# Optimization experiments

Measured on AMD Instinct MI355X. Metric: run time of the kernel, lower is better.

Reference implementation:

```python
import math
import jax, jax.numpy as jnp
from jax import lax
import numpy as np

B, N, D, H, L, F = 128, 200, 128, 8, 3, 2048


def setup_inputs():
    key = jax.random.key(0)
    ks = jax.random.split(key, 24)
    g = lambda i, shape: (0.05 * jax.random.normal(ks[i], shape)).astype(jnp.float32)
    coords = jax.random.uniform(ks[0], (B, N, 2), dtype=jnp.float32)
    demands = jax.random.uniform(ks[1], (B, N), minval=1.0, maxval=10.0, dtype=jnp.float32)
    demands = demands.at[:, 0].set(0.0)  # depot demand = 0
    capacity = jnp.full((B,), 50.0, jnp.float32)
    return dict(
        coords=coords, demands_raw=demands, capacity_raw=capacity,
        embed_W=g(2, (D, 3)), embed_b=g(3, (D,)),
        Wqkv=g(4, (L, 3 * D, D)), bqkv=g(5, (L, 3 * D)),
        Wo=g(6, (L, D, D)), bo=g(7, (L, D)),
        W1=g(8, (L, F, D)), b1=g(9, (L, F)),
        W2=g(10, (L, D, F)), b2=g(11, (L, D)),
        ln1_g=jnp.ones((L, D), jnp.float32), ln1_b=jnp.zeros((L, D), jnp.float32),
        ln2_g=jnp.ones((L, D), jnp.float32), ln2_b=jnp.zeros((L, D), jnp.float32),
        Wq=g(12, (D, D)), Wk=g(13, (D, D)),
        Wcap=g(14, (D, 1)), bcap=g(15, (D,)),
        Wctx=g(16, (D, 3 * D)), bctx=g(17, (D,)),
    )


def _ln(x, g, b):
    m = x.mean(-1, keepdims=True)
    v = ((x - m) ** 2).mean(-1, keepdims=True)
    return (x - m) / jnp.sqrt(v + 1e-5) * g + b


def _forward(coords, demands_raw, capacity_raw, embed_W, embed_b, Wqkv, bqkv, Wo, bo,
             W1, b1, W2, b2, ln1_g, ln1_b, ln2_g, ln2_b, Wq, Wk, Wcap, bcap, Wctx, bctx):
    Bd, Nd, _ = coords.shape
    cap = capacity_raw.reshape(Bd, 1)
    demand_ratio = demands_raw / cap                       # (B,N)
    x = jnp.concatenate([coords, demand_ratio[..., None]], -1)  # (B,N,3)
    h = x @ embed_W.T + embed_b                            # (B,N,D)
    d = h.shape[-1]
    dh = d // H
    # --- transformer encoder (post-LN, relu FFN), eval mode (no dropout) ---
    for i in range(Wqkv.shape[0]):
        qkv = h @ Wqkv[i].T + bqkv[i]
        q, k, v = jnp.split(qkv, 3, -1)
        q = q.reshape(Bd, Nd, H, dh)
        k = k.reshape(Bd, Nd, H, dh)
        v = v.reshape(Bd, Nd, H, dh)
        s = jnp.einsum('bqhd,bkhd->bhqk', q, k) / math.sqrt(dh)
        a = jax.nn.softmax(s, -1)
        o = jnp.einsum('bhqk,bkhd->bqhd', a, v).reshape(Bd, Nd, d) @ Wo[i].T + bo[i]
        h = _ln(h + o, ln1_g[i], ln1_b[i])
        f = jax.nn.relu(h @ W1[i].T + b1[i]) @ W2[i].T + b2[i]
        h = _ln(h + f, ln2_g[i], ln2_b[i])
    global_ctx = h.mean(1)                                 # (B,D)
    kmat = h @ Wk.T                                        # K cache: static across steps
    sqrt_d = math.sqrt(d)
    max_steps = 2 * (Nd - 1) + 1
    ar = jnp.arange(Bd)

    def step(carry, _):
        current, visited, remaining, done, key = carry
        key, sk = jax.random.split(key)
        cur_h = h[ar, current]                             # (B,D)
        cap_h = remaining @ Wcap.T + bcap                  # (B,D)
        q_in = jnp.concatenate([cur_h, global_ctx, cap_h], -1)
        q = (q_in @ Wctx.T + bctx) @ Wq.T                  # (B,D)
        logits = (kmat * q[:, None, :]).sum(-1) / sqrt_d   # (B,N)
        infeasible = visited | (demand_ratio > remaining)
        feas_cust = (~visited[:, 1:]) & (demand_ratio[:, 1:] <= remaining)
        has_feas = feas_cust.any(1)
        all_served = visited[:, 1:].all(1)
        force_depot = all_served & (current != 0) & (~done)
        at_depot = (current == 0) & (~done)
        not_depot = (current != 0) & (~done)
        # prevent_early_return=True path
        depot_mask = (at_depot & has_feas) | (not_depot & has_feas & (~all_served))
        infeasible = infeasible.at[:, 0].set(infeasible[:, 0] | depot_mask)
        force_depot = force_depot | (not_depot & (~has_feas)) | done
        masked = jnp.where(infeasible, -1e9, logits)
        logp = jax.nn.log_softmax(masked, -1)
        sel = jax.random.categorical(sk, masked)           # sampling decode
        sel_logp = logp[ar, sel]
        sel = jnp.where(force_depot, 0, sel)
        sel_logp = jnp.where(force_depot, 0.0, sel_logp)
        is_depot = sel == 0
        take = demand_ratio[ar, sel][:, None]
        remaining = jnp.clip(jnp.where(is_depot[:, None], 1.0, remaining - take), 0.0, 1.0)
        visited = visited.at[ar, sel].set(visited[ar, sel] | (~is_depot))
        done = done | (visited[:, 1:].all(1) & (sel == 0))
        return (sel, visited, remaining, done, key), (sel, sel_logp)

    init = (jnp.zeros(Bd, jnp.int32), jnp.zeros((Bd, Nd), bool),
            jnp.ones((Bd, 1), coords.dtype), jnp.zeros(Bd, bool), jax.random.key(42))
    _, (acts, lps) = lax.scan(step, init, None, length=max_steps)
    path = jnp.concatenate([jnp.zeros((Bd, 1), jnp.int32), acts.T], 1)  # (B, 1+max_steps)
    logps = lps.sum(0)                                                  # (B,)
    return path, logps


def reference(coords, demands_raw, capacity_raw, embed_W, embed_b, Wqkv, bqkv, Wo, bo,
              W1, b1, W2, b2, ln1_g, ln1_b, ln2_g, ln2_b, Wq, Wk, Wcap, bcap, Wctx, bctx):
    return _forward(coords, demands_raw, capacity_raw, embed_W, embed_b, Wqkv, bqkv, Wo, bo,
                    W1, b1, W2, b2, ln1_g, ln1_b, ln2_g, ln2_b, Wq, Wk, Wcap, bcap, Wctx, bctx)
```

## Files before the change

### kernel.cpp

```cpp
#include <hip/hip_runtime.h>
#include <hip/hip_bf16.h>
#include <stdint.h>
#include <math.h>

#define NB 128
#define NN 200
#define ND 128
#define NH 8
#define DH 16
#define NL 3
#define NF 2048
#define NT (NB * NN)
#define NSTEP 399

__host__ __device__ inline void tf2x32(unsigned k0, unsigned k1, unsigned x0, unsigned x1,
                                       unsigned* o0, unsigned* o1) {
  unsigned ks[3] = {k0, k1, k0 ^ k1 ^ 0x1BD11BDAu};
  x0 += ks[0]; x1 += ks[1];
  const unsigned R[2][4] = {{13u, 15u, 26u, 6u}, {17u, 29u, 16u, 24u}};
#pragma unroll
  for (int i = 0; i < 5; ++i) {
#pragma unroll
    for (int j = 0; j < 4; ++j) {
      unsigned r = R[i & 1][j];
      x0 += x1;
      x1 = (x1 << r) | (x1 >> (32u - r));
      x1 ^= x0;
    }
    x0 += ks[(i + 1) % 3];
    x1 += ks[(i + 2) % 3] + (unsigned)(i + 1);
  }
  *o0 = x0; *o1 = x1;
}

__global__ void k_rng(unsigned* __restrict__ rng) {
  __shared__ unsigned ksh[2 * NSTEP];
  const int l = threadIdx.x;
  if (l == 0) {
    unsigned k0 = 0u, k1 = 42u;
    for (int t = 0; t < NSTEP; ++t) {
      ksh[2 * t] = k0; ksh[2 * t + 1] = k1;
      unsigned a0, a1;
      tf2x32(k0, k1, 0u, 0u, &a0, &a1);
      k0 = a0; k1 = a1;
    }
  }
  __syncthreads();
  for (int t = l; t < NSTEP; t += 64) {
    unsigned s0, s1;
    tf2x32(ksh[2 * t], ksh[2 * t + 1], 0u, 1u, &s0, &s1);
    rng[2 * t] = s0; rng[2 * t + 1] = s1;
  }
}

__global__ __launch_bounds__(256) void k_gum(const unsigned* __restrict__ rng, float* __restrict__ gum) {
  int idx = blockIdx.x * 256 + threadIdx.x;
  if (idx >= NSTEP * NT) return;
  int t = idx / NT, j = idx - t * NT;
  unsigned o0, o1;
  tf2x32(rng[2 * t], rng[2 * t + 1], 0u, (unsigned)j, &o0, &o1);
  unsigned bits = o0 ^ o1;
  float u01 = __uint_as_float((bits >> 9) | 0x3f800000u) - 1.0f;
  float uu = fmaxf(1.17549435082228751e-38f, u01);
  gum[idx] = (float)(-log(-log((double)uu)));
}

__global__ void k_tr(const float* __restrict__ src, float* __restrict__ dst, int R, int C) {
  int i = blockIdx.x * 256 + threadIdx.x;
  if (i >= R * C) return;
  int c = i / R, r = i - c * R;
  dst[i] = src[(size_t)r * C + c];
}

__global__ void k_trd(const float* __restrict__ src, double* __restrict__ dst, int R, int C) {
  int i = blockIdx.x * 256 + threadIdx.x;
  if (i >= R * C) return;
  int c = i / R, r = i - c * R;
  dst[i] = (double)src[(size_t)r * C + c];
}

__global__ void k_embed(const float* __restrict__ coords, const float* __restrict__ dem,
                        const float* __restrict__ cap, const float* __restrict__ eW,
                        const float* __restrict__ eb, float* __restrict__ h, float* __restrict__ dr) {
  int gid = blockIdx.x * blockDim.x + threadIdx.x;
  int t = gid >> 7, d = gid & 127;
  int b = t / NN;
  float drv = dem[t] / cap[b];
  double acc = (double)eW[d * 3] * (double)coords[2 * t]
             + (double)eW[d * 3 + 1] * (double)coords[2 * t + 1]
             + (double)eW[d * 3 + 2] * (double)drv;
  h[gid] = (float)acc + eb[d];
  if (d == 0) dr[t] = drv;
}

#define QT 8
__global__ __launch_bounds__(384) void k_qkv(const float* __restrict__ h, const double* __restrict__ WT,
                                             const float* __restrict__ bias, float* __restrict__ qkv) {
  const int t0 = blockIdx.x * QT, j = threadIdx.x;
  __shared__ double hsh[ND][QT];
  for (int idx = j; idx < ND * QT; idx += 384) {
    int t = idx & 7, k = idx >> 3;
    hsh[k][t] = (double)h[(size_t)(t0 + t) * ND + k];
  }
  __syncthreads();
  double acc[QT];
#pragma unroll
  for (int t = 0; t < QT; ++t) acc[t] = 0.0;
  for (int k = 0; k < ND; ++k) {
    double w = WT[(size_t)k * 384 + j];
#pragma unroll
    for (int t = 0; t < QT; ++t) acc[t] += w * hsh[k][t];
  }
  float bv = bias[j];
#pragma unroll
  for (int t = 0; t < QT; ++t)
    qkv[(size_t)(t0 + t) * 384 + j] = (float)acc[t] + bv;
}

__global__ __launch_bounds__(256) void k_attn(const float* __restrict__ qkv, float* __restrict__ att) {
  const int b = blockIdx.x / NH, hh = blockIdx.x % NH, tid = threadIdx.x;
  const int lane = tid & 63, w = tid >> 6;
  __shared__ float qsh[NN][DH + 1];
  __shared__ float ksh[NN][DH + 1];
  __shared__ float vsh[NN][DH + 1];
  __shared__ float ashw[4][NN + 8];
  for (int idx = tid; idx < NN * DH; idx += 256) {
    int n = idx / DH, d2 = idx % DH;
    size_t base = (size_t)(b * NN + n) * 384 + hh * DH + d2;
    qsh[n][d2] = qkv[base];
    ksh[n][d2] = qkv[base + ND];
    vsh[n][d2] = qkv[base + 2 * ND];
  }
  __syncthreads();
  const int dd = lane & 15, q4 = lane >> 4;
  for (int qn = w; qn < NN; qn += 4) {
    double qv[DH];
#pragma unroll
    for (int d = 0; d < DH; ++d) qv[d] = (double)qsh[qn][d];
    float sf[4];
#pragma unroll
    for (int s = 0; s < 4; ++s) {
      int n = lane + 64 * s;
      if (n < NN) {
        double a = 0.0;
#pragma unroll
        for (int d = 0; d < DH; ++d) a += qv[d] * (double)ksh[n][d];
        sf[s] = (float)a / 4.0f;
      } else sf[s] = -3.0e38f;
    }
    float m = fmaxf(fmaxf(sf[0], sf[1]), fmaxf(sf[2], sf[3]));
    for (int off = 1; off < 64; off <<= 1) m = fmaxf(m, __shfl_xor(m, off, 64));
    double e[4];
    double esum = 0.0;
#pragma unroll
    for (int s = 0; s < 4; ++s) {
      int n = lane + 64 * s;
      e[s] = (n < NN) ? exp((double)(sf[s] - m)) : 0.0;
      esum += e[s];
    }
    for (int off = 1; off < 64; off <<= 1) esum += __shfl_xor(esum, off, 64);
#pragma unroll
    for (int s = 0; s < 4; ++s) {
      int n = lane + 64 * s;
      if (n < NN) ashw[w][n] = (float)(e[s] / esum);
    }
    double o = 0.0;
    for (int i = 0; i < 50; ++i) {
      int n = q4 * 50 + i;
      o += (double)ashw[w][n] * (double)vsh[n][dd];
    }
    o += __shfl_xor(o, 16, 64);
    o += __shfl_xor(o, 32, 64);
    if (lane < DH)
      att[(size_t)(b * NN + qn) * ND + hh * DH + lane] = (float)o;
  }
}

#define OT 4
__global__ __launch_bounds__(128) void k_oln(const float* __restrict__ att, const double* __restrict__ WoT,
                                             const float* __restrict__ bo, const float* __restrict__ g,
                                             const float* __restrict__ bb, const float* __restrict__ h,
                                             double* __restrict__ h64T) {
  const int t0 = blockIdx.x * OT, d = threadIdx.x;
  __shared__ double ash[ND][OT];
  __shared__ float xsh[OT][ND];
  __shared__ float mred[OT], sred[OT];
  for (int idx = d; idx < ND * OT; idx += 128) {
    int t = idx & 3, k = idx >> 2;
    ash[k][t] = (double)att[(size_t)(t0 + t) * ND + k];
  }
  __syncthreads();
  double acc[OT];
#pragma unroll
  for (int t = 0; t < OT; ++t) acc[t] = 0.0;
  for (int k = 0; k < ND; ++k) {
    double w = WoT[(size_t)k * ND + d];
#pragma unroll
    for (int t = 0; t < OT; ++t) acc[t] += w * ash[k][t];
  }
  float bv = bo[d];
#pragma unroll
  for (int t = 0; t < OT; ++t) {
    float o = (float)acc[t] + bv;
    xsh[t][d] = h[(size_t)(t0 + t) * ND + d] + o;
  }
  __syncthreads();
  if (d < OT) {
    double sv = 0.0;
    for (int k = 0; k < ND; ++k) sv += (double)xsh[d][k];
    float m = (float)(sv / 128.0);
    double sq = 0.0;
    for (int k = 0; k < ND; ++k) { float tf = xsh[d][k] - m; sq += (double)tf * (double)tf; }
    mred[d] = m;
    sred[d] = sqrtf((float)(sq / 128.0) + 1e-5f);
  }
  __syncthreads();
  const size_t blk8 = (size_t)(t0 >> 3);
  const int toff = t0 & 7;
#pragma unroll
  for (int t = 0; t < OT; ++t) {
    float tf = xsh[t][d] - mred[t];
    float hv = tf / sred[t] * g[d] + bb[d];
    h64T[blk8 * 1024 + (size_t)d * 8 + toff + t] = (double)hv;
  }
}

#define FT 8
__global__ __launch_bounds__(512, 4) void k_ffn(float* __restrict__ h, const double* __restrict__ h64T,
                                                const double* __restrict__ W1T, const float* __restrict__ b1,
                                                const float* __restrict__ W2T, const float* __restrict__ b2,
                                                const float* __restrict__ g, const float* __restrict__ bb) {
  const int tid = threadIdx.x;
  const int t0 = blockIdx.x * FT;
  const double* hp = h64T + (size_t)blockIdx.x * 1024;
  __shared__ double red_raw[NF * FT / 2];
  __shared__ float xsh[FT][ND];
  __shared__ float mred[FT], sred[FT];
  float* fsh32 = (float*)red_raw;
  {
    const int j0 = tid * 4;
    double acc[4][FT];
#pragma unroll
    for (int a = 0; a < 4; ++a)
#pragma unroll
      for (int t = 0; t < FT; ++t) acc[a][t] = 0.0;
    const double* wrow = W1T + j0;
    for (int k = 0; k < ND; ++k) {
      double2 wa = *(const double2*)(wrow + (size_t)k * NF);
      double2 wb = *(const double2*)(wrow + (size_t)k * NF + 2);
      double wd[4] = {wa.x, wa.y, wb.x, wb.y};
      const double* hr = hp + k * 8;
#pragma unroll
      for (int p = 0; p < 4; ++p) {
        double2 hv = *(const double2*)(hr + 2 * p);
#pragma unroll
        for (int a = 0; a < 4; ++a) {
          acc[a][2 * p] += wd[a] * hv.x;
          acc[a][2 * p + 1] += wd[a] * hv.y;
        }
      }
    }
#pragma unroll
    for (int a = 0; a < 4; ++a) {
      float bv = b1[j0 + a];
#pragma unroll
      for (int t = 0; t < FT; ++t) {
        float f = (float)acc[a][t] + bv;
        fsh32[(size_t)(j0 + a) * FT + t] = fmaxf(f, 0.0f);
      }
    }
  }
  __syncthreads();
  const int jg = tid >> 6;
  const int lane = tid & 63;
  const int th = lane >> 5;
  const int dlo = lane & 31, d0 = dlo << 2;
  double acc2[4][4];
#pragma unroll
  for (int a = 0; a < 4; ++a)
#pragma unroll
    for (int t = 0; t < 4; ++t) acc2[a][t] = 0.0;
  for (int c = 0; c < 2; ++c) {
    for (int i = 0; i < 128; ++i) {
      int jj = (jg << 7) | ((i + jg) & 127);
      int j = (c << 10) | jj;
      float4 wv = *(const float4*)(W2T + (size_t)j * ND + d0);
      float4 fq = *(const float4*)(fsh32 + (size_t)j * FT + th * 4);
      double fv[4] = {(double)fq.x, (double)fq.y, (double)fq.z, (double)fq.w};
      double wd[4] = {(double)wv.x, (double)wv.y, (double)wv.z, (double)wv.w};
#pragma unroll
      for (int a = 0; a < 4; ++a)
#pragma unroll
        for (int t = 0; t < 4; ++t) acc2[a][t] += wd[a] * fv[t];
    }
  }
  __syncthreads();
  double* red = red_raw;
#pragma unroll
  for (int a = 0; a < 4; ++a)
#pragma unroll
    for (int t = 0; t < 4; ++t)
      red[((jg * 8 + th * 4 + t) << 7) + d0 + a] = acc2[a][t];
  __syncthreads();
  for (int idx = tid; idx < ND * FT; idx += 512) {
    int t = idx >> 7, d = idx & 127;
    double s = 0.0;
#pragma unroll
    for (int jg2 = 0; jg2 < 8; ++jg2) s += red[((jg2 * 8 + t) << 7) + d];
    float o = (float)s + b2[d];
    float hres = (float)hp[(size_t)d * 8 + t];
    xsh[t][d] = hres + o;
  }
  __syncthreads();
  if (tid < FT) {
    double sv = 0.0;
    for (int d = 0; d < ND; ++d) sv += (double)xsh[tid][d];
    float m = (float)(sv / 128.0);
    double sq = 0.0;
    for (int d = 0; d < ND; ++d) { float tf = xsh[tid][d] - m; sq += (double)tf * (double)tf; }
    mred[tid] = m;
    sred[tid] = sqrtf((float)(sq / 128.0) + 1e-5f);
  }
  __syncthreads();
  for (int idx = tid; idx < ND * FT; idx += 512) {
    int d = idx & 127, t = idx >> 7;
    float tf = xsh[t][d] - mred[t];
    h[(size_t)(t0 + t) * ND + d] = tf / sred[t] * g[d] + bb[d];
  }
}

__global__ __launch_bounds__(128) void k_gctx(const float* __restrict__ h, float* __restrict__ gctx) {
  int b = blockIdx.x, d = threadIdx.x;
  double acc = 0.0;
  for (int n = 0; n < NN; ++n) acc += (double)h[(size_t)(b * NN + n) * ND + d];
  gctx[b * ND + d] = (float)(acc / 200.0);
}

#define KT 8
__global__ __launch_bounds__(128) void k_kmat(const float* __restrict__ h, const double* __restrict__ WkT,
                                              float* __restrict__ kmat) {
  const int t0 = blockIdx.x * KT, d = threadIdx.x;
  __shared__ double hsh[ND][KT];
  for (int idx = d; idx < ND * KT; idx += 128) {
    int t = idx & 7, k = idx >> 3;
    hsh[k][t] = (double)h[(size_t)(t0 + t) * ND + k];
  }
  __syncthreads();
  double acc[KT];
#pragma unroll
  for (int t = 0; t < KT; ++t) acc[t] = 0.0;
  for (int k = 0; k < ND; ++k) {
    double w = WkT[(size_t)k * ND + d];
#pragma unroll
    for (int t = 0; t < KT; ++t) acc[t] += w * hsh[k][t];
  }
#pragma unroll
  for (int t = 0; t < KT; ++t)
    kmat[(size_t)(t0 + t) * ND + d] = (float)acc[t];
}

__global__ __launch_bounds__(128) void k_prep1(const float* __restrict__ Wctx, const float* __restrict__ bcap,
                                               const float* __restrict__ Wcap, const float* __restrict__ bctx,
                                               double* __restrict__ t1, double* __restrict__ wu) {
  int k = threadIdx.x;
  double a = 0.0, c = 0.0;
  for (int m = 0; m < ND; ++m) {
    double wc = (double)Wctx[(size_t)k * 384 + 256 + m];
    a += wc * (double)bcap[m];
    c += wc * (double)Wcap[m];
  }
  t1[k] = a + (double)bctx[k];
  wu[k] = c;
}

__global__ __launch_bounds__(128) void k_M(const float* __restrict__ Wq, const float* __restrict__ Wctx,
                                           double* __restrict__ M) {
  int d = blockIdx.x, j = threadIdx.x;
  double acc = 0.0;
  for (int k = 0; k < ND; ++k)
    acc += (double)Wq[(size_t)d * ND + k] * (double)Wctx[(size_t)k * 384 + j];
  M[(size_t)d * ND + j] = acc;
}

__global__ __launch_bounds__(128) void k_u(const float* __restrict__ Wq, const double* __restrict__ wu,
                                           double* __restrict__ u) {
  int d = threadIdx.x;
  double acc = 0.0;
  for (int k = 0; k < ND; ++k) acc += (double)Wq[(size_t)d * ND + k] * wu[k];
  u[d] = acc;
}

__global__ __launch_bounds__(128) void k_t2(const float* __restrict__ Wctx, const float* __restrict__ gctx,
                                            double* __restrict__ t2) {
  int b = blockIdx.x, k = threadIdx.x;
  double acc = 0.0;
  for (int m = 0; m < ND; ++m)
    acc += (double)Wctx[(size_t)k * 384 + 128 + m] * (double)gctx[b * ND + m];
  t2[(size_t)b * ND + k] = acc;
}

__global__ __launch_bounds__(128) void k_vb(const float* __restrict__ Wq, const double* __restrict__ t2,
                                            const double* __restrict__ t1, double* __restrict__ vb) {
  int b = blockIdx.x, d = threadIdx.x;
  double acc = 0.0;
  for (int k = 0; k < ND; ++k)
    acc += (double)Wq[(size_t)d * ND + k] * (t2[(size_t)b * ND + k] + t1[k]);
  vb[(size_t)b * ND + d] = acc;
}

__global__ __launch_bounds__(256) void k_c01(const float* __restrict__ kmat, const double* __restrict__ vb,
                                             const double* __restrict__ u, float* __restrict__ c0, float* __restrict__ c1) {
  int t = blockIdx.x * 256 + threadIdx.x;
  if (t >= NT) return;
  int b = t / NN;
  double a0 = 0.0, a1 = 0.0;
  for (int d = 0; d < ND; ++d) {
    double km = (double)kmat[(size_t)t * ND + d];
    a0 += km * vb[(size_t)b * ND + d];
    a1 += km * u[d];
  }
  c0[t] = (float)a0;
  c1[t] = (float)a1;
}

__global__ __launch_bounds__(128) void k_KM(const float* __restrict__ kmat, const double* __restrict__ M,
                                            float* __restrict__ KMT) {
  const int t0 = blockIdx.x * KT, j = threadIdx.x;
  const int b = t0 / NN, toff = t0 % NN;
  __shared__ double ksh[ND][KT];
  for (int idx = j; idx < ND * KT; idx += 128) {
    int t = idx & 7, k = idx >> 3;
    ksh[k][t] = (double)kmat[(size_t)(t0 + t) * ND + k];
  }
  __syncthreads();
  double acc[KT];
#pragma unroll
  for (int t = 0; t < KT; ++t) acc[t] = 0.0;
  for (int d = 0; d < ND; ++d) {
    double m = M[(size_t)d * ND + j];
#pragma unroll
    for (int t = 0; t < KT; ++t) acc[t] += ksh[d][t] * m;
  }
#pragma unroll
  for (int t = 0; t < KT; ++t)
    KMT[(size_t)b * ND * NN + (size_t)j * NN + toff + t] = (float)acc[t];
}

#define PC 8
__global__ __launch_bounds__(256) void k_P(const float* __restrict__ KMT, const float* __restrict__ h,
                                           float* __restrict__ P) {
  const int blk = blockIdx.x;
  const int b = blk / 25, c0 = (blk % 25) * PC;
  const int tid = threadIdx.x;
  __shared__ double h8[ND][PC];
  for (int idx = tid; idx < ND * PC; idx += 256) {
    int t = idx & 7, j = idx >> 3;
    h8[j][t] = (double)h[(size_t)(b * NN + c0 + t) * ND + j];
  }
  __syncthreads();
  if (tid < NN) {
    double acc[PC];
#pragma unroll
    for (int t = 0; t < PC; ++t) acc[t] = 0.0;
    const float* kb = KMT + (size_t)b * ND * NN + tid;
    for (int j = 0; j < ND; ++j) {
      double km = (double)kb[(size_t)j * NN];
#pragma unroll
      for (int t = 0; t < PC; ++t) acc[t] += km * h8[j][t];
    }
#pragma unroll
    for (int t = 0; t < PC; ++t)
      P[(size_t)(b * NN + c0 + t) * NN + tid] = (float)acc[t];
  }
}

__global__ __launch_bounds__(64) void k_decode(const float* __restrict__ P, const float* __restrict__ c0,
                                               const float* __restrict__ c1, const float* __restrict__ dr,
                                               const float* __restrict__ gum, float* __restrict__ out) {
  __shared__ float Psh[NN * NN];
  const int b = blockIdx.x, l = threadIdx.x;
  {
    const float4* src = (const float4*)(P + (size_t)b * NN * NN);
    float4* dst = (float4*)Psh;
    for (int i = l; i < (NN * NN) / 4; i += 64) dst[i] = src[i];
  }
  float drs4[4], c04[4], c14[4];
  int vis4[4];
#pragma unroll
  for (int s = 0; s < 4; ++s) {
    int n = l + 64 * s;
    bool valid = n < NN;
    drs4[s] = valid ? dr[b * NN + n] : 1e9f;
    c04[s] = valid ? c0[b * NN + n] : 0.0f;
    c14[s] = valid ? c1[b * NN + n] : 0.0f;
    vis4[s] = valid ? 0 : 1;
  }
  int cur = 0, done = 0;
  float rem = 1.0f, lpsum = 0.0f;
  if (l == 0) out[(size_t)b * 400] = 0.0f;
  __syncthreads();
  const float SQD = 11.3137084989847603f;
  float gv4[4];
#pragma unroll
  for (int s = 0; s < 4; ++s) {
    int n = l + 64 * s;
    gv4[s] = (n < NN) ? gum[(size_t)0 * NT + b * NN + n] : 0.0f;
  }
  for (int t = 0; t < NSTEP; ++t) {
    float gn4[4];
    if (t + 1 < NSTEP) {
      const float* grow = gum + (size_t)(t + 1) * NT + b * NN;
#pragma unroll
      for (int s = 0; s < 4; ++s) {
        int n = l + 64 * s;
        gn4[s] = (n < NN) ? grow[n] : 0.0f;
      }
    }
    const float* Prow = Psh + cur * NN;
    float Pv4[4];
#pragma unroll
    for (int s = 0; s < 4; ++s) {
      int n = l + 64 * s;
      Pv4[s] = (n < NN) ? Prow[n] : 0.0f;
    }
    bool lf = false, lns = false;
#pragma unroll
    for (int s = 0; s < 4; ++s) {
      int n = l + 64 * s;
      if (n >= 1 && n < NN && !vis4[s]) {
        lns = true;
        if (drs4[s] <= rem) lf = true;
      }
    }
    const int has_feas = (__ballot(lf) != 0ULL);
    const int all_served = (__ballot(lns) == 0ULL);
    const bool at_depot = (cur == 0) && !done, not_depot = (cur != 0) && !done;
    const bool depot_mask = (at_depot && has_feas) || (not_depot && has_feas && !all_served);
    float msk[4], sc[4];
#pragma unroll
    for (int s = 0; s < 4; ++s) {
      int n = l + 64 * s;
      if (n < NN) {
        double sd = (double)Pv4[s] + (double)c04[s] + (double)rem * (double)c14[s];
        float logit = (float)sd / SQD;
        bool infn = vis4[s] || (drs4[s] > rem) || (n == 0 && depot_mask);
        msk[s] = infn ? -1e9f : logit;
        sc[s] = msk[s] + gv4[s];
      } else {
        msk[s] = -3.0e38f;
        sc[s] = -3.0e38f;
      }
    }
    float bs = sc[0]; int bn = l; float bmsk = msk[0]; float mx = msk[0];
#pragma unroll
    for (int s = 1; s < 4; ++s) {
      int n = l + 64 * s;
      if (sc[s] > bs) { bs = sc[s]; bn = n; bmsk = msk[s]; }
      mx = fmaxf(mx, msk[s]);
    }
    for (int off = 1; off < 64; off <<= 1) {
      float os = __shfl_xor(bs, off, 64);
      int on = __shfl_xor(bn, off, 64);
      float ob = __shfl_xor(bmsk, off, 64);
      float om = __shfl_xor(mx, off, 64);
      if (os > bs || (os == bs && on < bn)) { bs = os; bn = on; bmsk = ob; }
      mx = fmaxf(mx, om);
    }
    float e = 0.0f;
#pragma unroll
    for (int s = 0; s < 4; ++s) e += expf(msk[s] - mx);
    for (int off = 1; off < 64; off <<= 1) e += __shfl_xor(e, off, 64);
    int sel = bn;
    float slp = (bmsk - mx) - logf(e);
    bool force = (all_served && cur != 0 && !done) || (not_depot && !has_feas) || done;
    if (force) { sel = 0; slp = 0.0f; }
    if (l == 0) out[(size_t)b * 400 + 1 + t] = (float)sel;
    lpsum += slp;
    bool isd = (sel == 0);
    float cand = drs4[sel >> 6];
    float take = __shfl(cand, sel & 63, 64);
    float nr = isd ? 1.0f : (rem - take);
    rem = fminf(fmaxf(nr, 0.0f), 1.0f);
    if (!isd && (sel & 63) == l) vis4[sel >> 6] = 1;
    if (all_served && sel == 0) done = 1;
    cur = sel;
#pragma unroll
    for (int s = 0; s < 4; ++s) gv4[s] = gn4[s];
  }
  if (l == 0) out[(size_t)NB * 400 + b] = lpsum;
}

extern "C" void kernel_launch(void* const* d_in, const int* in_sizes, int n_in,
                              void* d_out, int out_size, void* d_ws, size_t ws_size,
                              hipStream_t stream) {
  (void)in_sizes; (void)n_in; (void)out_size; (void)ws_size;
  const float* coords = (const float*)d_in[0];
  const float* dem    = (const float*)d_in[1];
  const float* cap    = (const float*)d_in[2];
  const float* eW     = (const float*)d_in[3];
  const float* eb     = (const float*)d_in[4];
  const float* Wqkv   = (const float*)d_in[5];
  const float* bqkv   = (const float*)d_in[6];
  const float* Wo     = (const float*)d_in[7];
  const float* bo     = (const float*)d_in[8];
  const float* W1     = (const float*)d_in[9];
  const float* b1     = (const float*)d_in[10];
  const float* W2     = (const float*)d_in[11];
  const float* b2     = (const float*)d_in[12];
  const float* ln1g   = (const float*)d_in[13];
  const float* ln1b   = (const float*)d_in[14];
  const float* ln2g   = (const float*)d_in[15];
  const float* ln2b   = (const float*)d_in[16];
  const float* Wq     = (const float*)d_in[17];
  const float* Wk     = (const float*)d_in[18];
  const float* Wcap   = (const float*)d_in[19];
  const float* bcap   = (const float*)d_in[20];
  const float* Wctx   = (const float*)d_in[21];
  const float* bctx   = (const float*)d_in[22];

  char* ws = (char*)d_ws;
  size_t off = 0;
  auto take = [&](size_t bytes) -> void* {
    void* p = ws + off;
    off += (bytes + 255) & ~(size_t)255;
    return p;
  };
  float* dr   = (float*)take((size_t)NT * 4);
  float* c0   = (float*)take((size_t)NT * 4);
  float* c1   = (float*)take((size_t)NT * 4);
  float* P    = (float*)take((size_t)NB * NN * NN * 4);
  unsigned* rng = (unsigned*)take((size_t)NSTEP * 2 * 4);
  float* h    = (float*)take((size_t)NT * ND * 4);
  float* qkv  = (float*)take((size_t)NT * 384 * 4);
  float* att  = (float*)take((size_t)NT * ND * 4);
  float* kmat = (float*)take((size_t)NT * ND * 4);
  float* gctx = (float*)take((size_t)NB * ND * 4);
  double* M   = (double*)take((size_t)ND * ND * 8);
  double* u   = (double*)take((size_t)ND * 8);
  double* t1  = (double*)take((size_t)ND * 8);
  double* wu  = (double*)take((size_t)ND * 8);
  double* t2  = (double*)take((size_t)NB * ND * 8);
  double* vb  = (double*)take((size_t)NB * ND * 8);
  double* W1T   = (double*)take((size_t)NL * NF * ND * 8);
  float*  W2T   = (float*)take((size_t)NL * NF * ND * 4);
  double* WqkvT = (double*)take((size_t)NL * 384 * ND * 8);
  double* WoT   = (double*)take((size_t)NL * ND * ND * 8);
  double* WkT   = (double*)take((size_t)ND * ND * 8);
  double* h64T  = (double*)take((size_t)NT * ND * 8);
  float* KMT = qkv;
  float* gum = h;

  k_rng<<<1, 64, 0, stream>>>(rng);
  for (int i = 0; i < NL; ++i) {
    k_trd<<<(NF * ND + 255) / 256, 256, 0, stream>>>(W1 + (size_t)i * NF * ND, W1T + (size_t)i * NF * ND, NF, ND);
    k_tr<<<(NF * ND + 255) / 256, 256, 0, stream>>>(W2 + (size_t)i * ND * NF, W2T + (size_t)i * ND * NF, ND, NF);
    k_trd<<<(384 * ND + 255) / 256, 256, 0, stream>>>(Wqkv + (size_t)i * 384 * ND, WqkvT + (size_t)i * 384 * ND, 384, ND);
    k_trd<<<(ND * ND + 255) / 256, 256, 0, stream>>>(Wo + (size_t)i * ND * ND, WoT + (size_t)i * ND * ND, ND, ND);
  }
  k_trd<<<(ND * ND + 255) / 256, 256, 0, stream>>>(Wk, WkT, ND, ND);
  k_embed<<<(NT * ND) / 256, 256, 0, stream>>>(coords, dem, cap, eW, eb, h, dr);
  for (int i = 0; i < NL; ++i) {
    k_qkv<<<NT / QT, 384, 0, stream>>>(h, WqkvT + (size_t)i * 384 * ND, bqkv + (size_t)i * 384, qkv);
    k_attn<<<NB * NH, 256, 0, stream>>>(qkv, att);
    k_oln<<<NT / OT, 128, 0, stream>>>(att, WoT + (size_t)i * ND * ND, bo + (size_t)i * ND,
                                       ln1g + (size_t)i * ND, ln1b + (size_t)i * ND, h, h64T);
    k_ffn<<<NT / FT, 512, 0, stream>>>(h, h64T, W1T + (size_t)i * NF * ND, b1 + (size_t)i * NF,
                                       W2T + (size_t)i * ND * NF, b2 + (size_t)i * ND,
                                       ln2g + (size_t)i * ND, ln2b + (size_t)i * ND);
  }
  k_gctx<<<NB, 128, 0, stream>>>(h, gctx);
  k_kmat<<<NT / KT, 128, 0, stream>>>(h, WkT, kmat);
  k_prep1<<<1, 128, 0, stream>>>(Wctx, bcap, Wcap, bctx, t1, wu);
  k_M<<<ND, 128, 0, stream>>>(Wq, Wctx, M);
  k_u<<<1, 128, 0, stream>>>(Wq, wu, u);
  k_t2<<<NB, 128, 0, stream>>>(Wctx, gctx, t2);
  k_vb<<<NB, 128, 0, stream>>>(Wq, t2, t1, vb);
  k_c01<<<NT / 256, 256, 0, stream>>>(kmat, vb, u, c0, c1);
  k_KM<<<NT / KT, 128, 0, stream>>>(kmat, M, KMT);
  k_P<<<NB * 25, 256, 0, stream>>>(KMT, h, P);
  k_gum<<<(NSTEP * NT + 255) / 256, 256, 0, stream>>>(rng, gum);
  k_decode<<<NB, 64, 0, stream>>>(P, c0, c1, dr, gum, (float*)d_out);
}
```

Measured before the change: 4.724 ms.

## Feed GEMM kernels pre-transposed fp64 activations instead of staging through shared memory

Embed, attention and FFN now also write their outputs as tile-transposed double arrays (h64T, att64T), so qkv, output-projection and kmat kernels read per-k vectors straight from global memory and no longer stage through shared memory with a barrier. Attention keeps each lane's key rows in registers instead of re-reading shared memory for every query. The FFN hidden buffer becomes token-major with padding so the ReLU results go out as float4 stores. The extra fp64 writes add global traffic, and the register-held keys raise register pressure in attention.

```diff
diff --git a/kernel.cpp b/kernel.cpp
--- a/kernel.cpp
+++ b/kernel.cpp
@@ -81,7 +81,8 @@
 
 __global__ void k_embed(const float* __restrict__ coords, const float* __restrict__ dem,
                         const float* __restrict__ cap, const float* __restrict__ eW,
-                        const float* __restrict__ eb, float* __restrict__ h, float* __restrict__ dr) {
+                        const float* __restrict__ eb, float* __restrict__ h, float* __restrict__ dr,
+                        double* __restrict__ h64T) {
   int gid = blockIdx.x * blockDim.x + threadIdx.x;
   int t = gid >> 7, d = gid & 127;
   int b = t / NN;
@@ -89,27 +90,31 @@
   double acc = (double)eW[d * 3] * (double)coords[2 * t]
              + (double)eW[d * 3 + 1] * (double)coords[2 * t + 1]
              + (double)eW[d * 3 + 2] * (double)drv;
-  h[gid] = (float)acc + eb[d];
+  float hv = (float)acc + eb[d];
+  h[gid] = hv;
+  h64T[(size_t)(t >> 3) * 1024 + (size_t)d * 8 + (t & 7)] = (double)hv;
   if (d == 0) dr[t] = drv;
 }
 
 #define QT 8
-__global__ __launch_bounds__(384) void k_qkv(const float* __restrict__ h, const double* __restrict__ WT,
+__global__ __launch_bounds__(384) void k_qkv(const double* __restrict__ h64T, const double* __restrict__ WT,
                                              const float* __restrict__ bias, float* __restrict__ qkv) {
   const int t0 = blockIdx.x * QT, j = threadIdx.x;
-  __shared__ double hsh[ND][QT];
-  for (int idx = j; idx < ND * QT; idx += 384) {
-    int t = idx & 7, k = idx >> 3;
-    hsh[k][t] = (double)h[(size_t)(t0 + t) * ND + k];
-  }
-  __syncthreads();
+  const double* hp = h64T + (size_t)blockIdx.x * 1024;
   double acc[QT];
 #pragma unroll
   for (int t = 0; t < QT; ++t) acc[t] = 0.0;
   for (int k = 0; k < ND; ++k) {
     double w = WT[(size_t)k * 384 + j];
-#pragma unroll
-    for (int t = 0; t < QT; ++t) acc[t] += w * hsh[k][t];
+    const double* hr = hp + k * 8;
+    double2 h01 = *(const double2*)(hr);
+    double2 h23 = *(const double2*)(hr + 2);
+    double2 h45 = *(const double2*)(hr + 4);
+    double2 h67 = *(const double2*)(hr + 6);
+    acc[0] += w * h01.x; acc[1] += w * h01.y;
+    acc[2] += w * h23.x; acc[3] += w * h23.y;
+    acc[4] += w * h45.x; acc[5] += w * h45.y;
+    acc[6] += w * h67.x; acc[7] += w * h67.y;
   }
   float bv = bias[j];
 #pragma unroll
@@ -117,7 +122,7 @@
     qkv[(size_t)(t0 + t) * 384 + j] = (float)acc[t] + bv;
 }
 
-__global__ __launch_bounds__(256) void k_attn(const float* __restrict__ qkv, float* __restrict__ att) {
+__global__ __launch_bounds__(256) void k_attn(const float* __restrict__ qkv, double* __restrict__ att64T) {
   const int b = blockIdx.x / NH, hh = blockIdx.x % NH, tid = threadIdx.x;
   const int lane = tid & 63, w = tid >> 6;
   __shared__ float qsh[NN][DH + 1];
@@ -132,6 +137,18 @@
     vsh[n][d2] = qkv[base + 2 * ND];
   }
   __syncthreads();
+  float kreg[4][DH];
+#pragma unroll
+  for (int s = 0; s < 4; ++s) {
+    int n = lane + 64 * s;
+    if (n < NN) {
+#pragma unroll
+      for (int d = 0; d < DH; ++d) kreg[s][d] = ksh[n][d];
+    } else {
+#pragma unroll
+      for (int d = 0; d < DH; ++d) kreg[s][d] = 0.0f;
+    }
+  }
   const int dd = lane & 15, q4 = lane >> 4;
   for (int qn = w; qn < NN; qn += 4) {
     double qv[DH];
@@ -144,7 +161,7 @@
       if (n < NN) {
         double a = 0.0;
 #pragma unroll
-        for (int d = 0; d < DH; ++d) a += qv[d] * (double)ksh[n][d];
+        for (int d = 0; d < DH; ++d) a += qv[d] * (double)kreg[s][d];
         sf[s] = (float)a / 4.0f;
       } else sf[s] = -3.0e38f;
     }
@@ -171,32 +188,33 @@
     }
     o += __shfl_xor(o, 16, 64);
     o += __shfl_xor(o, 32, 64);
-    if (lane < DH)
-      att[(size_t)(b * NN + qn) * ND + hh * DH + lane] = (float)o;
+    if (lane < DH) {
+      int tq = b * NN + qn;
+      float of = (float)o;
+      att64T[(size_t)(tq >> 2) * 512 + (size_t)(hh * DH + lane) * 4 + (tq & 3)] = (double)of;
+    }
   }
 }
 
 #define OT 4
-__global__ __launch_bounds__(128) void k_oln(const float* __restrict__ att, const double* __restrict__ WoT,
+__global__ __launch_bounds__(128) void k_oln(const double* __restrict__ att64T, const double* __restrict__ WoT,
                                              const float* __restrict__ bo, const float* __restrict__ g,
                                              const float* __restrict__ bb, const float* __restrict__ h,
                                              double* __restrict__ h64T) {
   const int t0 = blockIdx.x * OT, d = threadIdx.x;
-  __shared__ double ash[ND][OT];
   __shared__ float xsh[OT][ND];
   __shared__ float mred[OT], sred[OT];
-  for (int idx = d; idx < ND * OT; idx += 128) {
-    int t = idx & 3, k = idx >> 2;
-    ash[k][t] = (double)att[(size_t)(t0 + t) * ND + k];
-  }
-  __syncthreads();
+  const double* ap = att64T + (size_t)blockIdx.x * 512;
   double acc[OT];
 #pragma unroll
   for (int t = 0; t < OT; ++t) acc[t] = 0.0;
   for (int k = 0; k < ND; ++k) {
     double w = WoT[(size_t)k * ND + d];
-#pragma unroll
-    for (int t = 0; t < OT; ++t) acc[t] += w * ash[k][t];
+    const double* ar = ap + k * 4;
+    double2 a01 = *(const double2*)(ar);
+    double2 a23 = *(const double2*)(ar + 2);
+    acc[0] += w * a01.x; acc[1] += w * a01.y;
+    acc[2] += w * a23.x; acc[3] += w * a23.y;
   }
   float bv = bo[d];
 #pragma unroll
@@ -226,14 +244,15 @@
 }
 
 #define FT 8
-__global__ __launch_bounds__(512, 4) void k_ffn(float* __restrict__ h, const double* __restrict__ h64T,
+#define FP 2056
+__global__ __launch_bounds__(512, 4) void k_ffn(float* __restrict__ h, double* __restrict__ h64T,
                                                 const double* __restrict__ W1T, const float* __restrict__ b1,
                                                 const float* __restrict__ W2T, const float* __restrict__ b2,
                                                 const float* __restrict__ g, const float* __restrict__ bb) {
   const int tid = threadIdx.x;
   const int t0 = blockIdx.x * FT;
   const double* hp = h64T + (size_t)blockIdx.x * 1024;
-  __shared__ double red_raw[NF * FT / 2];
+  __shared__ double red_raw[FT * FP / 2];
   __shared__ float xsh[FT][ND];
   __shared__ float mred[FT], sred[FT];
   float* fsh32 = (float*)red_raw;
@@ -260,14 +279,15 @@
         }
       }
     }
-#pragma unroll
-    for (int a = 0; a < 4; ++a) {
-      float bv = b1[j0 + a];
-#pragma unroll
-      for (int t = 0; t < FT; ++t) {
-        float f = (float)acc[a][t] + bv;
-        fsh32[(size_t)(j0 + a) * FT + t] = fmaxf(f, 0.0f);
-      }
+    float bv0 = b1[j0], bv1 = b1[j0 + 1], bv2 = b1[j0 + 2], bv3 = b1[j0 + 3];
+#pragma unroll
+    for (int t = 0; t < FT; ++t) {
+      float4 fw;
+      fw.x = fmaxf((float)acc[0][t] + bv0, 0.0f);
+      fw.y = fmaxf((float)acc[1][t] + bv1, 0.0f);
+      fw.z = fmaxf((float)acc[2][t] + bv2, 0.0f);
+      fw.w = fmaxf((float)acc[3][t] + bv3, 0.0f);
+      *(float4*)&fsh32[(size_t)t * FP + j0] = fw;
     }
   }
   __syncthreads();
@@ -285,8 +305,10 @@
       int jj = (jg << 7) | ((i + jg) & 127);
       int j = (c << 10) | jj;
       float4 wv = *(const float4*)(W2T + (size_t)j * ND + d0);
-      float4 fq = *(const float4*)(fsh32 + (size_t)j * FT + th * 4);
-      double fv[4] = {(double)fq.x, (double)fq.y, (double)fq.z, (double)fq.w};
+      double fv[4];
+#pragma unroll
+      for (int tt = 0; tt < 4; ++tt)
+        fv[tt] = (double)fsh32[(size_t)(th * 4 + tt) * FP + j];
       double wd[4] = {(double)wv.x, (double)wv.y, (double)wv.z, (double)wv.w};
 #pragma unroll
       for (int a = 0; a < 4; ++a)
@@ -325,7 +347,9 @@
   for (int idx = tid; idx < ND * FT; idx += 512) {
     int d = idx & 127, t = idx >> 7;
     float tf = xsh[t][d] - mred[t];
-    h[(size_t)(t0 + t) * ND + d] = tf / sred[t] * g[d] + bb[d];
+    float hv = tf / sred[t] * g[d] + bb[d];
+    h[(size_t)(t0 + t) * ND + d] = hv;
+    h64T[(size_t)blockIdx.x * 1024 + (size_t)d * 8 + t] = (double)hv;
   }
 }
 
@@ -337,22 +361,24 @@
 }
 
 #define KT 8
-__global__ __launch_bounds__(128) void k_kmat(const float* __restrict__ h, const double* __restrict__ WkT,
+__global__ __launch_bounds__(128) void k_kmat(const double* __restrict__ h64T, const double* __restrict__ WkT,
                                               float* __restrict__ kmat) {
   const int t0 = blockIdx.x * KT, d = threadIdx.x;
-  __shared__ double hsh[ND][KT];
-  for (int idx = d; idx < ND * KT; idx += 128) {
-    int t = idx & 7, k = idx >> 3;
-    hsh[k][t] = (double)h[(size_t)(t0 + t) * ND + k];
-  }
-  __syncthreads();
+  const double* hp = h64T + (size_t)blockIdx.x * 1024;
   double acc[KT];
 #pragma unroll
   for (int t = 0; t < KT; ++t) acc[t] = 0.0;
   for (int k = 0; k < ND; ++k) {
     double w = WkT[(size_t)k * ND + d];
-#pragma unroll
-    for (int t = 0; t < KT; ++t) acc[t] += w * hsh[k][t];
+    const double* hr = hp + k * 8;
+    double2 h01 = *(const double2*)(hr);
+    double2 h23 = *(const double2*)(hr + 2);
+    double2 h45 = *(const double2*)(hr + 4);
+    double2 h67 = *(const double2*)(hr + 6);
+    acc[0] += w * h01.x; acc[1] += w * h01.y;
+    acc[2] += w * h23.x; acc[3] += w * h23.y;
+    acc[4] += w * h45.x; acc[5] += w * h45.y;
+    acc[6] += w * h67.x; acc[7] += w * h67.y;
   }
 #pragma unroll
   for (int t = 0; t < KT; ++t)
@@ -632,7 +658,7 @@
   unsigned* rng = (unsigned*)take((size_t)NSTEP * 2 * 4);
   float* h    = (float*)take((size_t)NT * ND * 4);
   float* qkv  = (float*)take((size_t)NT * 384 * 4);
-  float* att  = (float*)take((size_t)NT * ND * 4);
+  double* att64T = (double*)take((size_t)NT * ND * 8);
   float* kmat = (float*)take((size_t)NT * ND * 4);
   float* gctx = (float*)take((size_t)NB * ND * 4);
   double* M   = (double*)take((size_t)ND * ND * 8);
@@ -658,18 +684,18 @@
     k_trd<<<(ND * ND + 255) / 256, 256, 0, stream>>>(Wo + (size_t)i * ND * ND, WoT + (size_t)i * ND * ND, ND, ND);
   }
   k_trd<<<(ND * ND + 255) / 256, 256, 0, stream>>>(Wk, WkT, ND, ND);
-  k_embed<<<(NT * ND) / 256, 256, 0, stream>>>(coords, dem, cap, eW, eb, h, dr);
+  k_embed<<<(NT * ND) / 256, 256, 0, stream>>>(coords, dem, cap, eW, eb, h, dr, h64T);
   for (int i = 0; i < NL; ++i) {
-    k_qkv<<<NT / QT, 384, 0, stream>>>(h, WqkvT + (size_t)i * 384 * ND, bqkv + (size_t)i * 384, qkv);
-    k_attn<<<NB * NH, 256, 0, stream>>>(qkv, att);
-    k_oln<<<NT / OT, 128, 0, stream>>>(att, WoT + (size_t)i * ND * ND, bo + (size_t)i * ND,
+    k_qkv<<<NT / QT, 384, 0, stream>>>(h64T, WqkvT + (size_t)i * 384 * ND, bqkv + (size_t)i * 384, qkv);
+    k_attn<<<NB * NH, 256, 0, stream>>>(qkv, att64T);
+    k_oln<<<NT / OT, 128, 0, stream>>>(att64T, WoT + (size_t)i * ND * ND, bo + (size_t)i * ND,
                                        ln1g + (size_t)i * ND, ln1b + (size_t)i * ND, h, h64T);
     k_ffn<<<NT / FT, 512, 0, stream>>>(h, h64T, W1T + (size_t)i * NF * ND, b1 + (size_t)i * NF,
                                        W2T + (size_t)i * ND * NF, b2 + (size_t)i * ND,
                                        ln2g + (size_t)i * ND, ln2b + (size_t)i * ND);
   }
   k_gctx<<<NB, 128, 0, stream>>>(h, gctx);
-  k_kmat<<<NT / KT, 128, 0, stream>>>(h, WkT, kmat);
+  k_kmat<<<NT / KT, 128, 0, stream>>>(h64T, WkT, kmat);
   k_prep1<<<1, 128, 0, stream>>>(Wctx, bcap, Wcap, bctx, t1, wu);
   k_M<<<ND, 128, 0, stream>>>(Wq, Wctx, M);
   k_u<<<1, 128, 0, stream>>>(Wq, wu, u);
```

New measurement: 4.902 ms. +3.8%, slower.
